# Optimization experiments

Hardware: AMD Instinct MI355X
Metric: run time of the kernel (lower is better)

Reference implementation:

```python
import jax, jax.numpy as jnp
import numpy as np

B, C_IN, C_OUT, K, H, W = 8, 64, 64, 3, 128, 128
CTX = max(8, C_OUT // 4)  # 16


def setup_inputs() -> dict:
    key = jax.random.key(0)
    ks = jax.random.split(key, 6)
    x = jax.random.normal(ks[0], (B, C_IN, H, W), dtype=jnp.float32)
    # context_proj: 1x1 conv (ctx_ch, C_in) + bias
    ctx_w = jax.random.normal(ks[1], (CTX, C_IN), dtype=jnp.float32) * (1.0 / np.sqrt(C_IN))
    ctx_b = jnp.zeros((CTX,), dtype=jnp.float32)
    # kernel_gen: Linear(ctx_ch -> C_out*C_in*K*K), init std=0.001, zero bias
    kg_w = jax.random.normal(ks[2], (C_OUT * C_IN * K * K, CTX), dtype=jnp.float32) * 0.001
    kg_b = jnp.zeros((C_OUT * C_IN * K * K,), dtype=jnp.float32)
    gamma = jnp.zeros((C_OUT,), dtype=jnp.float32)
    bias = jnp.zeros((C_OUT,), dtype=jnp.float32)
    # value_proj: 1x1 conv (C_in, C_in), no bias
    value_w = jax.random.normal(ks[3], (C_IN, C_IN), dtype=jnp.float32) * (1.0 / np.sqrt(C_IN))
    return {"x": x, "ctx_w": ctx_w, "ctx_b": ctx_b, "kg_w": kg_w, "kg_b": kg_b,
            "gamma": gamma, "bias": bias, "value_w": value_w}


def reference(x, ctx_w, ctx_b, kg_w, kg_b, gamma, bias, value_w):
    b = x.shape[0]
    # context projection (1x1 conv) + global average pool -> (B, CTX)
    ctx = jnp.einsum('bchw,oc->bohw', x, ctx_w) + ctx_b[None, :, None, None]
    ctx_vec = jnp.mean(ctx, axis=(2, 3))  # (B, CTX)
    # per-sample kernel generation
    kernels_flat = ctx_vec @ kg_w.T + kg_b  # (B, O*C*K*K)
    kernels = jnp.tanh(kernels_flat.reshape(b, C_OUT, C_IN, K, K))
    mean_k = jnp.mean(kernels.reshape(b, C_OUT, -1), axis=-1)  # (B, O)
    lam = jax.nn.sigmoid(gamma)[None, :, None, None, None]
    kernels = kernels - lam * mean_k[:, :, None, None, None]
    # value projection (1x1 conv, no bias)
    v = jnp.einsum('bchw,oc->bohw', x, value_w)
    # unfold: patches (B, C*K*K, H, W), feature order (C, kh, kw) matching F.unfold
    pad = K // 2
    patches = jax.lax.conv_general_dilated_patches(
        v, filter_shape=(K, K), window_strides=(1, 1),
        padding=[(pad, pad), (pad, pad)])  # (B, C*K*K, H, W)
    out = jnp.einsum('bof,bfhw->bohw', kernels.reshape(b, C_OUT, -1), patches)
    out = out + bias[None, :, None, None]
    return jax.nn.relu(out)
```

## Files before the change

### kernel.cpp

```cpp
#include <hip/hip_runtime.h>
#include <stdint.h>

#define NB 8
#define CIN 64
#define COUT 64
#define HH 128
#define WW 128

typedef unsigned short ushort_t;
typedef unsigned int uint_t;
typedef __attribute__((ext_vector_type(8))) __bf16 bf16x8;
typedef __attribute__((ext_vector_type(4))) float f32x4;

__device__ __forceinline__ ushort_t f2bf(float f) {
  uint_t u = __builtin_bit_cast(uint_t, f);
  u += 0x7fffu + ((u >> 16) & 1u);
  return (ushort_t)(u >> 16);
}

#define WS_XSUM 0
#define WS_XT   2048
#define WS_A    16779264

__global__ void k_zero(float* p) {
  int i = blockIdx.x * 256 + threadIdx.x;
  if (i < 512) p[i] = 0.f;
}

__global__ void k_trans(const float* __restrict__ x, ushort_t* __restrict__ xT,
                        float* __restrict__ xsum) {
  __shared__ float tile[64 * 129];
  int b = blockIdx.x >> 7;
  int h = blockIdx.x & 127;
  int tid = threadIdx.x;
  int w = tid & 127;
  int ch = tid >> 7;
  const float* xp = x + ((size_t)(b * 64) * 128 + h) * 128 + w;
#pragma unroll
  for (int p = 0; p < 32; ++p) {
    int c = p * 2 + ch;
    tile[c * 129 + w] = xp[(size_t)c * 16384];
  }
  __syncthreads();
  if (tid < 64) {
    float s = 0.f;
#pragma unroll 8
    for (int w2 = 0; w2 < 128; ++w2) s += tile[tid * 129 + w2];
    atomicAdd(&xsum[b * 64 + tid], s);
  }
#pragma unroll
  for (int it = 0; it < 4; ++it) {
    int chunk = tid + it * 256;
    int w2 = chunk >> 3;
    int cc = chunk & 7;
    union { ushort_t u[8]; int4 v; } pk;
#pragma unroll
    for (int j = 0; j < 8; ++j) pk.u[j] = f2bf(tile[(cc * 8 + j) * 129 + w2]);
    *reinterpret_cast<int4*>(xT + (((size_t)(b * 128 + h) * 128 + w2) * 64 + cc * 8)) = pk.v;
  }
}

__global__ void k_gen(const float* __restrict__ xsum,
                      const float* __restrict__ ctx_w, const float* __restrict__ ctx_b,
                      const float* __restrict__ kg_w, const float* __restrict__ kg_b,
                      const float* __restrict__ gamma, const float* __restrict__ value_w,
                      ushort_t* __restrict__ A) {
  __shared__ float xm[64];
  __shared__ float ctxv[16];
  __shared__ float ks_[576];
  __shared__ float red[256];
  __shared__ float vw[4096];
  int b = blockIdx.x >> 6;
  int o = blockIdx.x & 63;
  int tid = threadIdx.x;
  if (tid < 64) xm[tid] = xsum[b * 64 + tid] * (1.f / 16384.f);
#pragma unroll
  for (int p = 0; p < 16; ++p) vw[tid + p * 256] = value_w[tid + p * 256];
  __syncthreads();
  if (tid < 16) {
    float s = ctx_b[tid];
#pragma unroll 8
    for (int c = 0; c < 64; ++c) s += xm[c] * ctx_w[tid * 64 + c];
    ctxv[tid] = s;
  }
  __syncthreads();
  float val[3] = {0.f, 0.f, 0.f};
  float partial = 0.f;
#pragma unroll
  for (int p = 0; p < 3; ++p) {
    int i = tid + p * 256;
    if (i < 576) {
      int n = o * 576 + i;
      float s = kg_b[n];
      const float* kwp = kg_w + (size_t)n * 16;
#pragma unroll
      for (int j = 0; j < 16; ++j) s += ctxv[j] * kwp[j];
      val[p] = tanhf(s);
      partial += val[p];
    }
  }
  red[tid] = partial;
  __syncthreads();
  for (int s = 128; s > 0; s >>= 1) {
    if (tid < s) red[tid] += red[tid + s];
    __syncthreads();
  }
  float mean = red[0] * (1.f / 576.f);
  float lam = 1.f / (1.f + expf(-gamma[o]));
#pragma unroll
  for (int p = 0; p < 3; ++p) {
    int i = tid + p * 256;
    if (i < 576) ks_[i] = val[p] - lam * mean;
  }
  __syncthreads();
  ushort_t* Ao = A + (size_t)(b * 64 + o) * 576;
#pragma unroll
  for (int p = 0; p < 3; ++p) {
    int f = tid + p * 256;
    if (f < 576) {
      int tap = f >> 6;
      int c = f & 63;
      float s = 0.f;
#pragma unroll 8
      for (int cp = 0; cp < 64; ++cp) s += ks_[cp * 9 + tap] * vw[cp * 64 + c];
      Ao[f] = f2bf(s);
    }
  }
}

__launch_bounds__(256)
__global__ void k_conv(const ushort_t* __restrict__ xT, const ushort_t* __restrict__ A,
                       const float* __restrict__ bias, float* __restrict__ out) {
  __shared__ __align__(16) ushort_t xs[6 * 34 * 72];
  int bx = blockIdx.x;
  int b = bx >> 7;
  int rem = bx & 127;
  int h0 = (rem >> 2) * 4;
  int w0 = (rem & 3) * 32;
  int tid = threadIdx.x;
  int wave = tid >> 6;
  int lane = tid & 63;
  int n16 = lane & 15;
  int q = lane >> 4;

  bf16x8 af[18];
  const ushort_t* Ag = A + (size_t)(b * 64 + wave * 16 + n16) * 576 + q * 8;
#pragma unroll
  for (int ks = 0; ks < 18; ++ks)
    af[ks] = *reinterpret_cast<const bf16x8*>(Ag + ks * 32);

  const ushort_t* xb = xT + (size_t)b * 128 * 128 * 64;
#pragma unroll
  for (int it = 0; it < 7; ++it) {
    int chunk = tid + it * 256;
    if (chunk < 1632) {
      int lr = chunk / 272;
      int r2 = chunk - lr * 272;
      int lc = r2 >> 3;
      int cc = r2 & 7;
      int hh = h0 - 1 + lr;
      int ww = w0 - 1 + lc;
      int4 v = make_int4(0, 0, 0, 0);
      if (hh >= 0 && hh < 128 && ww >= 0 && ww < 128)
        v = *reinterpret_cast<const int4*>(xb + ((size_t)(hh * 128 + ww) * 64 + cc * 8));
      *reinterpret_cast<int4*>(xs + ((lr * 34 + lc) * 72 + cc * 8)) = v;
    }
  }
  __syncthreads();

  f32x4 acc[8];
#pragma unroll
  for (int i = 0; i < 8; ++i) acc[i] = (f32x4){0.f, 0.f, 0.f, 0.f};

  const ushort_t* xsl = xs + n16 * 72 + q * 8;
#pragma unroll
  for (int rr = 0; rr < 4; ++rr) {
#pragma unroll
    for (int cb = 0; cb < 2; ++cb) {
      int nt = rr * 2 + cb;
#pragma unroll
      for (int tap = 0; tap < 9; ++tap) {
        int kh = tap / 3, kw2 = tap % 3;
#pragma unroll
        for (int cq = 0; cq < 2; ++cq) {
          bf16x8 bf = *reinterpret_cast<const bf16x8*>(
              xsl + ((rr + kh) * 34 + cb * 16 + kw2) * 72 + cq * 32);
          acc[nt] = __builtin_amdgcn_mfma_f32_16x16x32_bf16(af[tap * 2 + cq], bf, acc[nt], 0, 0, 0);
        }
      }
    }
  }

#pragma unroll
  for (int rr = 0; rr < 4; ++rr) {
#pragma unroll
    for (int cb = 0; cb < 2; ++cb) {
      int nt = rr * 2 + cb;
      int hcur = h0 + rr;
      int wcur = w0 + cb * 16 + n16;
#pragma unroll
      for (int r = 0; r < 4; ++r) {
        int o = wave * 16 + q * 4 + r;
        float v = acc[nt][r] + bias[o];
        v = fmaxf(v, 0.f);
        out[((size_t)(b * 64 + o) * 128 + hcur) * 128 + wcur] = v;
      }
    }
  }
}

extern "C" void kernel_launch(void* const* d_in, const int* in_sizes, int n_in,
                              void* d_out, int out_size, void* d_ws, size_t ws_size,
                              hipStream_t stream) {
  const float* x       = (const float*)d_in[0];
  const float* ctx_w   = (const float*)d_in[1];
  const float* ctx_b   = (const float*)d_in[2];
  const float* kg_w    = (const float*)d_in[3];
  const float* kg_b    = (const float*)d_in[4];
  const float* gamma   = (const float*)d_in[5];
  const float* bias    = (const float*)d_in[6];
  const float* value_w = (const float*)d_in[7];
  float* out = (float*)d_out;

  float* xsum  = (float*)((char*)d_ws + WS_XSUM);
  ushort_t* xT = (ushort_t*)((char*)d_ws + WS_XT);
  ushort_t* A  = (ushort_t*)((char*)d_ws + WS_A);

  k_zero<<<2, 256, 0, stream>>>(xsum);
  k_trans<<<1024, 256, 0, stream>>>(x, xT, xsum);
  k_gen<<<512, 256, 0, stream>>>(xsum, ctx_w, ctx_b, kg_w, kg_b, gamma, value_w, A);
  k_conv<<<1024, 256, 0, stream>>>(xT, A, bias, out);
}
```

Baseline: 126.1 us.

## Drop atomic zeroing kernel and retile conv waves for B-fragment reuse

Each transpose block now writes its per-row channel sums to a partial buffer, and the generator kernel reduces them. This removes the separate zeroing launch and the atomics. The conv kernel gives each wave 32 output channels over 4 pixel tiles instead of 16 channels over 8 tiles, so each LDS B-fragment load feeds two MFMAs. That doubles the A-fragment registers, and the launch bounds now request 2 blocks per CU, which raises the risk of register spills.

```diff
diff --git a/kernel.cpp b/kernel.cpp
--- a/kernel.cpp
+++ b/kernel.cpp
@@ -18,17 +18,12 @@
   return (ushort_t)(u >> 16);
 }
 
-#define WS_XSUM 0
-#define WS_XT   2048
-#define WS_A    16779264
-
-__global__ void k_zero(float* p) {
-  int i = blockIdx.x * 256 + threadIdx.x;
-  if (i < 512) p[i] = 0.f;
-}
+#define WS_PART 0
+#define WS_XT   262144
+#define WS_A    17039360
 
 __global__ void k_trans(const float* __restrict__ x, ushort_t* __restrict__ xT,
-                        float* __restrict__ xsum) {
+                        float* __restrict__ part) {
   __shared__ float tile[64 * 129];
   int b = blockIdx.x >> 7;
   int h = blockIdx.x & 127;
@@ -46,7 +41,7 @@
     float s = 0.f;
 #pragma unroll 8
     for (int w2 = 0; w2 < 128; ++w2) s += tile[tid * 129 + w2];
-    atomicAdd(&xsum[b * 64 + tid], s);
+    part[((size_t)b * 128 + h) * 64 + tid] = s;
   }
 #pragma unroll
   for (int it = 0; it < 4; ++it) {
@@ -60,7 +55,7 @@
   }
 }
 
-__global__ void k_gen(const float* __restrict__ xsum,
+__global__ void k_gen(const float* __restrict__ part,
                       const float* __restrict__ ctx_w, const float* __restrict__ ctx_b,
                       const float* __restrict__ kg_w, const float* __restrict__ kg_b,
                       const float* __restrict__ gamma, const float* __restrict__ value_w,
@@ -73,9 +68,20 @@
   int b = blockIdx.x >> 6;
   int o = blockIdx.x & 63;
   int tid = threadIdx.x;
-  if (tid < 64) xm[tid] = xsum[b * 64 + tid] * (1.f / 16384.f);
+  {
+    int c = tid & 63;
+    int g = tid >> 6;
+    float s = 0.f;
+    const float* pp = part + ((size_t)b * 128 + g * 32) * 64 + c;
+#pragma unroll 8
+    for (int h = 0; h < 32; ++h) s += pp[h * 64];
+    red[tid] = s;
+  }
 #pragma unroll
   for (int p = 0; p < 16; ++p) vw[tid + p * 256] = value_w[tid + p * 256];
+  __syncthreads();
+  if (tid < 64)
+    xm[tid] = (red[tid] + red[tid + 64] + red[tid + 128] + red[tid + 192]) * (1.f / 16384.f);
   __syncthreads();
   if (tid < 16) {
     float s = ctx_b[tid];
@@ -99,6 +105,7 @@
       partial += val[p];
     }
   }
+  __syncthreads();
   red[tid] = partial;
   __syncthreads();
   for (int s = 128; s > 0; s >>= 1) {
@@ -128,7 +135,7 @@
   }
 }
 
-__launch_bounds__(256)
+__launch_bounds__(256, 2)
 __global__ void k_conv(const ushort_t* __restrict__ xT, const ushort_t* __restrict__ A,
                        const float* __restrict__ bias, float* __restrict__ out) {
   __shared__ __align__(16) ushort_t xs[6 * 34 * 72];
@@ -142,12 +149,17 @@
   int lane = tid & 63;
   int n16 = lane & 15;
   int q = lane >> 4;
-
-  bf16x8 af[18];
-  const ushort_t* Ag = A + (size_t)(b * 64 + wave * 16 + n16) * 576 + q * 8;
-#pragma unroll
-  for (int ks = 0; ks < 18; ++ks)
-    af[ks] = *reinterpret_cast<const bf16x8*>(Ag + ks * 32);
+  int p  = wave & 1;
+  int oh = wave >> 1;
+
+  bf16x8 af[2][18];
+#pragma unroll
+  for (int t = 0; t < 2; ++t) {
+    const ushort_t* Ag = A + (size_t)(b * 64 + oh * 32 + t * 16 + n16) * 576 + q * 8;
+#pragma unroll
+    for (int ks = 0; ks < 18; ++ks)
+      af[t][ks] = *reinterpret_cast<const bf16x8*>(Ag + ks * 32);
+  }
 
   const ushort_t* xb = xT + (size_t)b * 128 * 128 * 64;
 #pragma unroll
@@ -168,40 +180,43 @@
   }
   __syncthreads();
 
-  f32x4 acc[8];
-#pragma unroll
-  for (int i = 0; i < 8; ++i) acc[i] = (f32x4){0.f, 0.f, 0.f, 0.f};
+  f32x4 acc[4][2];
+#pragma unroll
+  for (int i = 0; i < 4; ++i)
+#pragma unroll
+    for (int t = 0; t < 2; ++t) acc[i][t] = (f32x4){0.f, 0.f, 0.f, 0.f};
 
   const ushort_t* xsl = xs + n16 * 72 + q * 8;
 #pragma unroll
-  for (int rr = 0; rr < 4; ++rr) {
-#pragma unroll
-    for (int cb = 0; cb < 2; ++cb) {
-      int nt = rr * 2 + cb;
-#pragma unroll
-      for (int tap = 0; tap < 9; ++tap) {
-        int kh = tap / 3, kw2 = tap % 3;
-#pragma unroll
-        for (int cq = 0; cq < 2; ++cq) {
-          bf16x8 bf = *reinterpret_cast<const bf16x8*>(
-              xsl + ((rr + kh) * 34 + cb * 16 + kw2) * 72 + cq * 32);
-          acc[nt] = __builtin_amdgcn_mfma_f32_16x16x32_bf16(af[tap * 2 + cq], bf, acc[nt], 0, 0, 0);
-        }
+  for (int pt = 0; pt < 4; ++pt) {
+    int nt = p * 4 + pt;
+    int rr = nt >> 1, cb = nt & 1;
+#pragma unroll
+    for (int tap = 0; tap < 9; ++tap) {
+      int kh = tap / 3, kw2 = tap % 3;
+#pragma unroll
+      for (int cq = 0; cq < 2; ++cq) {
+        bf16x8 bf = *reinterpret_cast<const bf16x8*>(
+            xsl + ((rr + kh) * 34 + cb * 16 + kw2) * 72 + cq * 32);
+        int ks = tap * 2 + cq;
+        acc[pt][0] = __builtin_amdgcn_mfma_f32_16x16x32_bf16(af[0][ks], bf, acc[pt][0], 0, 0, 0);
+        acc[pt][1] = __builtin_amdgcn_mfma_f32_16x16x32_bf16(af[1][ks], bf, acc[pt][1], 0, 0, 0);
       }
     }
   }
 
 #pragma unroll
-  for (int rr = 0; rr < 4; ++rr) {
-#pragma unroll
-    for (int cb = 0; cb < 2; ++cb) {
-      int nt = rr * 2 + cb;
-      int hcur = h0 + rr;
-      int wcur = w0 + cb * 16 + n16;
+  for (int pt = 0; pt < 4; ++pt) {
+    int nt = p * 4 + pt;
+    int rr = nt >> 1, cb = nt & 1;
+    int hcur = h0 + rr;
+    int wcur = w0 + cb * 16 + n16;
+#pragma unroll
+    for (int t = 0; t < 2; ++t) {
 #pragma unroll
       for (int r = 0; r < 4; ++r) {
-        int o = wave * 16 + q * 4 + r;
-        float v = acc[nt][r] + bias[o];
+        int o = oh * 32 + t * 16 + q * 4 + r;
+        float v = acc[pt][t][r] + bias[o];
         v = fmaxf(v, 0.f);
         out[((size_t)(b * 64 + o) * 128 + hcur) * 128 + wcur] = v;
       }
@@ -222,12 +237,11 @@
   const float* value_w = (const float*)d_in[7];
   float* out = (float*)d_out;
 
-  float* xsum  = (float*)((char*)d_ws + WS_XSUM);
+  float* part  = (float*)((char*)d_ws + WS_PART);
   ushort_t* xT = (ushort_t*)((char*)d_ws + WS_XT);
   ushort_t* A  = (ushort_t*)((char*)d_ws + WS_A);
 
-  k_zero<<<2, 256, 0, stream>>>(xsum);
-  k_trans<<<1024, 256, 0, stream>>>(x, xT, xsum);
-  k_gen<<<512, 256, 0, stream>>>(xsum, ctx_w, ctx_b, kg_w, kg_b, gamma, value_w, A);
+  k_trans<<<1024, 256, 0, stream>>>(x, xT, part);
+  k_gen<<<512, 256, 0, stream>>>(part, ctx_w, ctx_b, kg_w, kg_b, gamma, value_w, A);
   k_conv<<<1024, 256, 0, stream>>>(xT, A, bias, out);
 }
```

Measured after the change: 132.0 us. 4.7% more time.
